# Kernel tuning notes

Measured on AMD Instinct MI355X. Metric: run time of the kernel, lower is better.

## Reference

```python
import jax, jax.numpy as jnp
import numpy as np

N, IN_DIM, HID, OUT_DIM = 50000, 32, 128, 10
NUM_LAYERS = 4
K = NUM_LAYERS + 1          # max hop
E_K = 400000                # edges per hop level (k_idx blocks are contiguous, equal-sized)
G = 500                     # number of graphs in the batch
N_CONVS = sum(l + 1 for l in range(NUM_LAYERS + 1))  # 15


def setup_inputs() -> dict:
    key = jax.random.key(0)
    ks = jax.random.split(key, 8)
    x = jax.random.normal(ks[0], (N, IN_DIM), jnp.float32)
    k_edge_index = jax.random.randint(ks[1], (2, K * E_K), 0, N)
    # hop label per edge, sorted so hop k occupies the static slice [(k-1)*E_K : k*E_K]
    k_idx = jnp.repeat(jnp.arange(1, K + 1), E_K)
    # sorted graph ids, every graph non-empty (~100 nodes each)
    batch = jnp.sort(jnp.arange(N) % G)
    emb_W = jax.random.normal(ks[2], (HID, IN_DIM), jnp.float32) * 0.05
    emb_b = jnp.zeros((HID,), jnp.float32)
    conv_W = jax.random.normal(ks[3], (N_CONVS, HID, HID), jnp.float32) * 0.05
    conv_b = jnp.zeros((N_CONVS, HID), jnp.float32)
    r1_W = jax.random.normal(ks[4], (HID * 3 // 2, HID * 3), jnp.float32) * 0.05
    r1_b = jnp.zeros((HID * 3 // 2,), jnp.float32)
    r2_W = jax.random.normal(ks[5], (OUT_DIM, HID * 3 // 2), jnp.float32) * 0.05
    r2_b = jnp.zeros((OUT_DIM,), jnp.float32)
    return {"x": x, "k_edge_index": k_edge_index, "k_idx": k_idx, "batch": batch,
            "emb_W": emb_W, "emb_b": emb_b, "conv_W": conv_W, "conv_b": conv_b,
            "r1_W": r1_W, "r1_b": r1_b, "r2_W": r2_W, "r2_b": r2_b}


def _gcn_conv(h_in, W, b, src, dst):
    # PyG GCNConv: h = x W^T; add self-loops; sym-normalized scatter-add; + bias
    h = h_in @ W.T                                   # [N, HID]
    deg = jnp.zeros((N,), h.dtype).at[dst].add(1.0) + 1.0   # in-degree + self-loop
    dinv = jax.lax.rsqrt(deg)                        # deg >= 1 always
    coef = dinv[src] * dinv[dst]                     # [E_K]
    msg = h[src] * coef[:, None]                     # gather + scale
    agg = jnp.zeros_like(h).at[dst].add(msg)         # scatter-add
    return agg + (dinv * dinv)[:, None] * h + b      # self-loop term + bias


def _forward(x, k_edge_index, k_idx, batch, emb_W, emb_b, conv_W, conv_b,
             r1_W, r1_b, r2_W, r2_b):
    h = x @ emb_W.T + emb_b
    x_l = [h]
    ci = 0
    for l in range(NUM_LAYERS + 1):
        x_k = None
        for k in range(1, l + 2):
            # static slice == k_edge_index[:, k_idx == k] (k_idx blocks are contiguous)
            src = k_edge_index[0, (k - 1) * E_K: k * E_K]
            dst = k_edge_index[1, (k - 1) * E_K: k * E_K]
            inp = h if k == 1 else x_l[-k]           # delayed residual input
            term = _gcn_conv(inp, conv_W[ci], conv_b[ci], src, dst) / k
            x_k = term if k == 1 else x_k + term
            ci += 1
        h = jax.nn.relu(x_k)
        x_l.append(h)
    # global add / max / mean pooling over graphs
    ssum = jax.ops.segment_sum(h, batch, num_segments=G)
    smax = jax.ops.segment_max(h, batch, num_segments=G)
    cnt = jax.ops.segment_sum(jnp.ones((N,), h.dtype), batch, num_segments=G)
    smean = ssum / jnp.maximum(cnt, 1.0)[:, None]
    pooled = jnp.concatenate([ssum, smax, smean], axis=1)   # [G, 3*HID]
    hid = jax.nn.leaky_relu(pooled @ r1_W.T + r1_b, 0.01)
    return hid @ r2_W.T + r2_b                               # [G, OUT_DIM]


def reference(x, k_edge_index, k_idx, batch, emb_W, emb_b, conv_W, conv_b,
              r1_W, r1_b, r2_W, r2_b):
    return _forward(x, k_edge_index, k_idx, batch, emb_W, emb_b, conv_W, conv_b,
                    r1_W, r1_b, r2_W, r2_b)
```

## Files before the change

### kernel.cpp

```cpp
#include <hip/hip_runtime.h>
#include <cstdint>
#include <cstddef>

#define NN 50000
#define INDIM 32
#define HIDD 128
#define OUTD 10
#define KK 5
#define EK 400000
#define GG 500
#define CAP 40

typedef __attribute__((ext_vector_type(4))) float float4v;
typedef __attribute__((ext_vector_type(4))) unsigned short ushort4v;
typedef unsigned short ushort;

__global__ void k_scatter(const int* __restrict__ srcA, const int* __restrict__ dstA,
                          int* __restrict__ cnt, ushort* __restrict__ col) {
    int e = blockIdx.x * blockDim.x + threadIdx.x;
    if (e >= KK * EK) return;
    int s = e / EK;
    int sv = srcA[e], dv = dstA[e];
    int pos = atomicAdd(&cnt[s * NN + dv], 1);
    if (pos < CAP) col[(size_t)(s * NN + dv) * CAP + pos] = (ushort)sv;
}

__global__ void k_dinv(const int* __restrict__ cnt, float* __restrict__ dinv,
                       float* __restrict__ dinv2s) {
    int i = blockIdx.x * blockDim.x + threadIdx.x;
    if (i >= KK * NN) return;
    int s = i / NN;
    float d = (float)(cnt[i] + 1);
    dinv[i]   = 1.0f / sqrtf(d);
    dinv2s[i] = 1.0f / (d * (float)(s + 1));
}

__global__ void k_tr(const float* __restrict__ in, float* __restrict__ out,
                     int J, int C, int total) {
    int idx = blockIdx.x * blockDim.x + threadIdx.x;
    if (idx >= total) return;
    int jc = J * C;
    int m = idx / jc, rem = idx - m * jc;
    int j = rem / C, c = rem - j * C;
    out[m * jc + c * J + j] = in[idx];
}

__global__ __launch_bounds__(256) void k_layer(const float* __restrict__ xl,
                                               const int* __restrict__ cnt,
                                               const ushort* __restrict__ col,
                                               const float* __restrict__ dinv,
                                               const float* __restrict__ dinv2s,
                                               const float* __restrict__ Wt,
                                               const float* __restrict__ conv_b,
                                               int lp1, float* __restrict__ out) {
    constexpr int LDA = HIDD + 4;
    __shared__ float At[64 * LDA];
    const int tid = threadIdx.x;
    const int r0 = blockIdx.x * 64;
    const int lane = tid & 63, wv = tid >> 6;
    const int half = lane >> 5, ln = lane & 31;
    const int tr = tid >> 4, tc = tid & 15;
    const int ra = tr * 4;
    const int cib = (lp1 - 1) * lp1 / 2;

    float acc[4][8];
#pragma unroll
    for (int q = 0; q < 4; ++q)
#pragma unroll
        for (int u = 0; u < 8; ++u) acc[q][u] = 0.f;

    for (int k = 1; k <= lp1; ++k) {
        const int s = k - 1, sN = s * NN, ci = cib + s;
        const float inv_k = 1.0f / (float)k;
        const float* Xin = xl + (size_t)(lp1 - k) * NN * HIDD;

#pragma unroll 1
        for (int pass = 0; pass < 8; ++pass) {
            int lrow = pass * 8 + wv * 2 + half;
            int node = r0 + lrow;
            bool valid = node < NN;
            int nc = valid ? node : NN - 1;
            int cn = 0;
            if (valid) {
                cn = cnt[sN + node];
                cn = cn < CAP ? cn : CAP;
            }
            const ushort* cp = col + (size_t)(sN + nc) * CAP;
            float hd = valid ? dinv[sN + node] * inv_k : 0.f;
            float sd = valid ? dinv2s[sN + node] : 0.f;
            const float* Xb = Xin + ln * 4;
            float4v a = (*(const float4v*)(Xb + (size_t)nc * HIDD)) * sd;

            int cm = cn;
            {
                int o = __shfl_xor(cn, 32);
                cm = cm > o ? cm : o;
            }
            for (int i = 0; i < cm; i += 4) {
                ushort4v cc = *(const ushort4v*)(cp + i);
                int j0 = (i + 0 < cn) ? (int)cc.x : nc;
                int j1 = (i + 1 < cn) ? (int)cc.y : nc;
                int j2 = (i + 2 < cn) ? (int)cc.z : nc;
                int j3 = (i + 3 < cn) ? (int)cc.w : nc;
                float w0 = dinv[sN + j0] * hd;
                float w1 = dinv[sN + j1] * hd;
                float w2 = dinv[sN + j2] * hd;
                float w3 = dinv[sN + j3] * hd;
                if (i + 0 >= cn) w0 = 0.f;
                if (i + 1 >= cn) w1 = 0.f;
                if (i + 2 >= cn) w2 = 0.f;
                if (i + 3 >= cn) w3 = 0.f;
                float4v x0 = *(const float4v*)(Xb + (size_t)j0 * HIDD);
                float4v x1 = *(const float4v*)(Xb + (size_t)j1 * HIDD);
                float4v x2 = *(const float4v*)(Xb + (size_t)j2 * HIDD);
                float4v x3 = *(const float4v*)(Xb + (size_t)j3 * HIDD);
                a += x0 * w0 + x1 * w1 + x2 * w2 + x3 * w3;
            }
            *(float4v*)(&At[lrow * LDA + ln * 4]) = a;
        }
        __syncthreads();

        const float* wp = Wt + (size_t)ci * HIDD * HIDD + tc * 8;
#pragma unroll 4
        for (int c = 0; c < HIDD; ++c) {
            float4v w0 = *(const float4v*)(wp + (size_t)c * HIDD);
            float4v w1 = *(const float4v*)(wp + (size_t)c * HIDD + 4);
            float a0 = At[(ra + 0) * LDA + c];
            float a1 = At[(ra + 1) * LDA + c];
            float a2 = At[(ra + 2) * LDA + c];
            float a3 = At[(ra + 3) * LDA + c];
#pragma unroll
            for (int u = 0; u < 4; ++u) {
                acc[0][u] += a0 * w0[u];  acc[0][u + 4] += a0 * w1[u];
                acc[1][u] += a1 * w0[u];  acc[1][u + 4] += a1 * w1[u];
                acc[2][u] += a2 * w0[u];  acc[2][u + 4] += a2 * w1[u];
                acc[3][u] += a3 * w0[u];  acc[3][u + 4] += a3 * w1[u];
            }
        }
        __syncthreads();
    }

    float bj[8];
#pragma unroll
    for (int u = 0; u < 8; ++u) bj[u] = 0.f;
    for (int k = 1; k <= lp1; ++k) {
        const float* bp = conv_b + (size_t)(cib + k - 1) * HIDD + tc * 8;
        float inv_k = 1.0f / (float)k;
#pragma unroll
        for (int u = 0; u < 8; ++u) bj[u] += bp[u] * inv_k;
    }
#pragma unroll
    for (int q = 0; q < 4; ++q) {
        int gr = r0 + ra + q;
        if (gr >= NN) continue;
        float* op = out + (size_t)gr * HIDD + tc * 8;
        float4v o0, o1;
#pragma unroll
        for (int u = 0; u < 4; ++u) {
            float v0 = acc[q][u] + bj[u];
            float v1 = acc[q][u + 4] + bj[u + 4];
            o0[u] = v0 > 0.f ? v0 : 0.f;
            o1[u] = v1 > 0.f ? v1 : 0.f;
        }
        *(float4v*)(op) = o0;
        *(float4v*)(op + 4) = o1;
    }
}

__global__ __launch_bounds__(256) void k_emb(const float* __restrict__ A,
                                             const float* __restrict__ Wt,
                                             const float* __restrict__ bias,
                                             float* __restrict__ out) {
    constexpr int KD = INDIM, LDA = KD + 4;
    __shared__ float At[64 * LDA];
    int tid = threadIdx.x;
    int r0 = blockIdx.x * 64;

    constexpr int F4R = KD / 4;
    constexpr int PER = 64 * F4R / 256;
#pragma unroll
    for (int t = 0; t < PER; ++t) {
        int f4 = tid + t * 256;
        int row = f4 / F4R, c4 = (f4 - row * F4R) * 4;
        float4v v = {0.f, 0.f, 0.f, 0.f};
        int gr = r0 + row;
        if (gr < NN) v = *(const float4v*)(A + (size_t)gr * KD + c4);
        *(float4v*)(At + row * LDA + c4) = v;
    }
    __syncthreads();

    int tr = tid >> 4, tc = tid & 15;
    int ra = tr * 4;
    float acc[4][8];
#pragma unroll
    for (int q = 0; q < 4; ++q)
#pragma unroll
        for (int u = 0; u < 8; ++u) acc[q][u] = 0.f;

    const float* wp = Wt + tc * 8;
#pragma unroll
    for (int c = 0; c < KD; ++c) {
        float4v w0 = *(const float4v*)(wp + (size_t)c * HIDD);
        float4v w1 = *(const float4v*)(wp + (size_t)c * HIDD + 4);
        float a0 = At[(ra + 0) * LDA + c];
        float a1 = At[(ra + 1) * LDA + c];
        float a2 = At[(ra + 2) * LDA + c];
        float a3 = At[(ra + 3) * LDA + c];
#pragma unroll
        for (int u = 0; u < 4; ++u) {
            acc[0][u] += a0 * w0[u];  acc[0][u + 4] += a0 * w1[u];
            acc[1][u] += a1 * w0[u];  acc[1][u + 4] += a1 * w1[u];
            acc[2][u] += a2 * w0[u];  acc[2][u + 4] += a2 * w1[u];
            acc[3][u] += a3 * w0[u];  acc[3][u + 4] += a3 * w1[u];
        }
    }

#pragma unroll
    for (int q = 0; q < 4; ++q) {
        int gr = r0 + ra + q;
        if (gr >= NN) continue;
        float* op = out + (size_t)gr * HIDD + tc * 8;
        float4v o0, o1;
#pragma unroll
        for (int u = 0; u < 4; ++u) {
            o0[u] = acc[q][u] + bias[tc * 8 + u];
            o1[u] = acc[q][u + 4] + bias[tc * 8 + u + 4];
        }
        *(float4v*)(op) = o0;
        *(float4v*)(op + 4) = o1;
    }
}

__global__ __launch_bounds__(256) void k_poolf(const float* __restrict__ h,
                                               const float* __restrict__ r1W,
                                               const float* __restrict__ r1b,
                                               const float* __restrict__ r2W,
                                               const float* __restrict__ r2b,
                                               float* __restrict__ out) {
    __shared__ float pooled[384];
    __shared__ float hid[192];
    int g = blockIdx.x, tid = threadIdx.x;
    if (tid < 128) {
        const float* hp = h + (size_t)g * 100 * HIDD + tid;
        float s = 0.f, m = -3.0e38f;
        for (int n = 0; n < 100; ++n) {
            float v = hp[(size_t)n * HIDD];
            s += v;
            m = fmaxf(m, v);
        }
        pooled[tid] = s;
        pooled[128 + tid] = m;
        pooled[256 + tid] = s * 0.01f;
    }
    __syncthreads();
    if (tid < 192) {
        float acc = r1b[tid];
        const float* w = r1W + (size_t)tid * 384;
        for (int c = 0; c < 384; ++c) acc += pooled[c] * w[c];
        hid[tid] = acc >= 0.f ? acc : 0.01f * acc;
    }
    __syncthreads();
    if (tid < OUTD) {
        float acc = r2b[tid];
        const float* w = r2W + (size_t)tid * 192;
        for (int c = 0; c < 192; ++c) acc += hid[c] * w[c];
        out[g * OUTD + tid] = acc;
    }
}

extern "C" void kernel_launch(void* const* d_in, const int* in_sizes, int n_in,
                              void* d_out, int out_size, void* d_ws, size_t ws_size,
                              hipStream_t stream) {
    const float* x      = (const float*)d_in[0];
    const int*   kei    = (const int*)d_in[1];
    const float* emb_W  = (const float*)d_in[4];
    const float* emb_b  = (const float*)d_in[5];
    const float* conv_W = (const float*)d_in[6];
    const float* conv_b = (const float*)d_in[7];
    const float* r1W    = (const float*)d_in[8];
    const float* r1b    = (const float*)d_in[9];
    const float* r2W    = (const float*)d_in[10];
    const float* r2b    = (const float*)d_in[11];

    const int* srcA = kei;
    const int* dstA = kei + KK * EK;

    char* p = (char*)d_ws;
    auto take = [&](size_t bytes) -> void* {
        void* q = (void*)p;
        p += (bytes + 255) & ~(size_t)255;
        return q;
    };
    int*    cnt    = (int*)   take((size_t)KK * NN * 4);
    float*  dinv   = (float*) take((size_t)KK * NN * 4);
    float*  dinv2s = (float*) take((size_t)KK * NN * 4);
    ushort* col    = (ushort*)take((size_t)KK * NN * CAP * 2);
    float*  Wt     = (float*) take((size_t)15 * HIDD * HIDD * 4);
    float*  embWt  = (float*) take((size_t)INDIM * HIDD * 4);
    float*  xl     = (float*) take((size_t)6 * NN * HIDD * 4);

    hipMemsetAsync(cnt, 0, (size_t)KK * NN * 4, stream);

    int etotal = KK * EK;
    k_scatter<<<(etotal + 255) / 256, 256, 0, stream>>>(srcA, dstA, cnt, col);
    k_dinv<<<(KK * NN + 255) / 256, 256, 0, stream>>>(cnt, dinv, dinv2s);

    k_tr<<<(15 * HIDD * HIDD + 255) / 256, 256, 0, stream>>>(conv_W, Wt, HIDD, HIDD,
                                                             15 * HIDD * HIDD);
    k_tr<<<(HIDD * INDIM + 255) / 256, 256, 0, stream>>>(emb_W, embWt, HIDD, INDIM,
                                                         HIDD * INDIM);

    k_emb<<<(NN + 63) / 64, 256, 0, stream>>>(x, embWt, emb_b, xl);

    for (int l = 0; l < 5; ++l) {
        k_layer<<<(NN + 63) / 64, 256, 0, stream>>>(
            xl, cnt, col, dinv, dinv2s, Wt, conv_b, l + 1,
            xl + (size_t)(l + 1) * NN * HIDD);
    }

    k_poolf<<<GG, 256, 0, stream>>>(xl + (size_t)5 * NN * HIDD, r1W, r1b, r2W, r2b,
                                    (float*)d_out);
}
```

Before: 1.215 ms.

## Halve layer tile to 32 rows, prefetch neighbor indices, fold dinv scaling

The fused layer kernel now processes 32 nodes per block instead of 64. This doubles the grid, halves the shared tile and accumulator registers, and is meant to raise occupancy and latency hiding for the irregular gathers. The gather loop prefetches the next block of neighbor indices and issues feature loads before the dinv loads. The destination's dinv and 1/k are factored out of the loop and applied once, which removes the separate dinv2s array and its kernel output. In exchange, each block reloads the weight matrix for half as many rows, and the index prefetch reads past each row, so the col buffer is padded.

```diff
diff --git a/kernel.cpp b/kernel.cpp
--- a/kernel.cpp
+++ b/kernel.cpp
@@ -25,14 +25,11 @@
     if (pos < CAP) col[(size_t)(s * NN + dv) * CAP + pos] = (ushort)sv;
 }
 
-__global__ void k_dinv(const int* __restrict__ cnt, float* __restrict__ dinv,
-                       float* __restrict__ dinv2s) {
+__global__ void k_dinv(const int* __restrict__ cnt, float* __restrict__ dinv) {
     int i = blockIdx.x * blockDim.x + threadIdx.x;
     if (i >= KK * NN) return;
-    int s = i / NN;
     float d = (float)(cnt[i] + 1);
-    dinv[i]   = 1.0f / sqrtf(d);
-    dinv2s[i] = 1.0f / (d * (float)(s + 1));
+    dinv[i] = 1.0f / sqrtf(d);
 }
 
 __global__ void k_tr(const float* __restrict__ in, float* __restrict__ out,
@@ -49,23 +46,22 @@
                                                const int* __restrict__ cnt,
                                                const ushort* __restrict__ col,
                                                const float* __restrict__ dinv,
-                                               const float* __restrict__ dinv2s,
                                                const float* __restrict__ Wt,
                                                const float* __restrict__ conv_b,
                                                int lp1, float* __restrict__ out) {
     constexpr int LDA = HIDD + 4;
-    __shared__ float At[64 * LDA];
+    __shared__ float At[32 * LDA];
     const int tid = threadIdx.x;
-    const int r0 = blockIdx.x * 64;
+    const int r0 = blockIdx.x * 32;
     const int lane = tid & 63, wv = tid >> 6;
     const int half = lane >> 5, ln = lane & 31;
     const int tr = tid >> 4, tc = tid & 15;
-    const int ra = tr * 4;
+    const int ra = tr * 2;
     const int cib = (lp1 - 1) * lp1 / 2;
 
-    float acc[4][8];
-#pragma unroll
-    for (int q = 0; q < 4; ++q)
+    float acc[2][8];
+#pragma unroll
+    for (int q = 0; q < 2; ++q)
 #pragma unroll
         for (int u = 0; u < 8; ++u) acc[q][u] = 0.f;
 
@@ -73,9 +69,10 @@
         const int s = k - 1, sN = s * NN, ci = cib + s;
         const float inv_k = 1.0f / (float)k;
         const float* Xin = xl + (size_t)(lp1 - k) * NN * HIDD;
+        const float* dvs = dinv + sN;
 
 #pragma unroll 1
-        for (int pass = 0; pass < 8; ++pass) {
+        for (int pass = 0; pass < 4; ++pass) {
             int lrow = pass * 8 + wv * 2 + half;
             int node = r0 + lrow;
             bool valid = node < NN;
@@ -86,37 +83,40 @@
                 cn = cn < CAP ? cn : CAP;
             }
             const ushort* cp = col + (size_t)(sN + nc) * CAP;
-            float hd = valid ? dinv[sN + node] * inv_k : 0.f;
-            float sd = valid ? dinv2s[sN + node] : 0.f;
+            float dv = valid ? dvs[node] : 0.f;
+            float hd = dv * inv_k;
             const float* Xb = Xin + ln * 4;
-            float4v a = (*(const float4v*)(Xb + (size_t)nc * HIDD)) * sd;
-
-            int cm = cn;
+            float4v apart = (*(const float4v*)(Xb + (size_t)nc * HIDD)) * dv;
+
+            int cnr = (cn + 3) & ~3;
+            int cm = cnr;
             {
-                int o = __shfl_xor(cn, 32);
+                int o = __shfl_xor(cnr, 32);
                 cm = cm > o ? cm : o;
             }
+            ushort4v cc = *(const ushort4v*)(cp);
             for (int i = 0; i < cm; i += 4) {
-                ushort4v cc = *(const ushort4v*)(cp + i);
+                ushort4v ccn = *(const ushort4v*)(cp + i + 4);
                 int j0 = (i + 0 < cn) ? (int)cc.x : nc;
                 int j1 = (i + 1 < cn) ? (int)cc.y : nc;
                 int j2 = (i + 2 < cn) ? (int)cc.z : nc;
                 int j3 = (i + 3 < cn) ? (int)cc.w : nc;
-                float w0 = dinv[sN + j0] * hd;
-                float w1 = dinv[sN + j1] * hd;
-                float w2 = dinv[sN + j2] * hd;
-                float w3 = dinv[sN + j3] * hd;
+                float4v x0 = *(const float4v*)(Xb + (size_t)j0 * HIDD);
+                float4v x1 = *(const float4v*)(Xb + (size_t)j1 * HIDD);
+                float4v x2 = *(const float4v*)(Xb + (size_t)j2 * HIDD);
+                float4v x3 = *(const float4v*)(Xb + (size_t)j3 * HIDD);
+                float w0 = dvs[j0];
+                float w1 = dvs[j1];
+                float w2 = dvs[j2];
+                float w3 = dvs[j3];
                 if (i + 0 >= cn) w0 = 0.f;
                 if (i + 1 >= cn) w1 = 0.f;
                 if (i + 2 >= cn) w2 = 0.f;
                 if (i + 3 >= cn) w3 = 0.f;
-                float4v x0 = *(const float4v*)(Xb + (size_t)j0 * HIDD);
-                float4v x1 = *(const float4v*)(Xb + (size_t)j1 * HIDD);
-                float4v x2 = *(const float4v*)(Xb + (size_t)j2 * HIDD);
-                float4v x3 = *(const float4v*)(Xb + (size_t)j3 * HIDD);
-                a += x0 * w0 + x1 * w1 + x2 * w2 + x3 * w3;
+                apart += x0 * w0 + x1 * w1 + x2 * w2 + x3 * w3;
+                cc = ccn;
             }
-            *(float4v*)(&At[lrow * LDA + ln * 4]) = a;
+            *(float4v*)(&At[lrow * LDA + ln * 4]) = apart * hd;
         }
         __syncthreads();
 
@@ -127,14 +127,10 @@
             float4v w1 = *(const float4v*)(wp + (size_t)c * HIDD + 4);
             float a0 = At[(ra + 0) * LDA + c];
             float a1 = At[(ra + 1) * LDA + c];
-            float a2 = At[(ra + 2) * LDA + c];
-            float a3 = At[(ra + 3) * LDA + c];
 #pragma unroll
             for (int u = 0; u < 4; ++u) {
                 acc[0][u] += a0 * w0[u];  acc[0][u + 4] += a0 * w1[u];
                 acc[1][u] += a1 * w0[u];  acc[1][u + 4] += a1 * w1[u];
-                acc[2][u] += a2 * w0[u];  acc[2][u + 4] += a2 * w1[u];
-                acc[3][u] += a3 * w0[u];  acc[3][u + 4] += a3 * w1[u];
             }
         }
         __syncthreads();
@@ -150,7 +146,7 @@
         for (int u = 0; u < 8; ++u) bj[u] += bp[u] * inv_k;
     }
 #pragma unroll
-    for (int q = 0; q < 4; ++q) {
+    for (int q = 0; q < 2; ++q) {
         int gr = r0 + ra + q;
         if (gr >= NN) continue;
         float* op = out + (size_t)gr * HIDD + tc * 8;
@@ -293,8 +289,7 @@
     };
     int*    cnt    = (int*)   take((size_t)KK * NN * 4);
     float*  dinv   = (float*) take((size_t)KK * NN * 4);
-    float*  dinv2s = (float*) take((size_t)KK * NN * 4);
-    ushort* col    = (ushort*)take((size_t)KK * NN * CAP * 2);
+    ushort* col    = (ushort*)take((size_t)KK * NN * CAP * 2 + 64);
     float*  Wt     = (float*) take((size_t)15 * HIDD * HIDD * 4);
     float*  embWt  = (float*) take((size_t)INDIM * HIDD * 4);
     float*  xl     = (float*) take((size_t)6 * NN * HIDD * 4);
@@ -303,7 +298,7 @@
 
     int etotal = KK * EK;
     k_scatter<<<(etotal + 255) / 256, 256, 0, stream>>>(srcA, dstA, cnt, col);
-    k_dinv<<<(KK * NN + 255) / 256, 256, 0, stream>>>(cnt, dinv, dinv2s);
+    k_dinv<<<(KK * NN + 255) / 256, 256, 0, stream>>>(cnt, dinv);
 
     k_tr<<<(15 * HIDD * HIDD + 255) / 256, 256, 0, stream>>>(conv_W, Wt, HIDD, HIDD,
                                                              15 * HIDD * HIDD);
@@ -313,8 +308,8 @@
     k_emb<<<(NN + 63) / 64, 256, 0, stream>>>(x, embWt, emb_b, xl);
 
     for (int l = 0; l < 5; ++l) {
-        k_layer<<<(NN + 63) / 64, 256, 0, stream>>>(
-            xl, cnt, col, dinv, dinv2s, Wt, conv_b, l + 1,
+        k_layer<<<(NN + 31) / 32, 256, 0, stream>>>(
+            xl, cnt, col, dinv, Wt, conv_b, l + 1,
             xl + (size_t)(l + 1) * NN * HIDD);
     }
 
```

New measurement: 1.416 ms. +16.5%, slower.
